# Performance work log

Hardware: AMD Instinct MI355X
Metric: run time of the kernel (lower is better)

The kernel has to match this reference:

```python
import jax, jax.numpy as jnp
import numpy as np

B, N, S, NS = 16, 4096, 512, 32
RADIUS = 0.4
EPS = 1e-5
CHANS = [6, 64, 64, 128]


def setup_inputs() -> dict:
    key = jax.random.key(0)
    ks = jax.random.split(key, 8)
    inp = {
        "xyz": jax.random.normal(ks[0], (B, 3, N), jnp.float32),
        "points": jax.random.normal(ks[1], (B, 3, N), jnp.float32),
    }
    for i in range(3):
        cin, cout = CHANS[i], CHANS[i + 1]
        inp[f"w{i}"] = jax.random.normal(ks[2 + i], (cout, cin), jnp.float32) * (1.0 / np.sqrt(cin))
        inp[f"b{i}"] = jnp.zeros((cout,), jnp.float32)
        inp[f"g{i}"] = jnp.ones((cout,), jnp.float32)
        inp[f"beta{i}"] = jnp.zeros((cout,), jnp.float32)
    return inp


def _fps(xyz):
    # xyz: [B, N, 3] -> indices [B, S] (deterministic start at index 0)
    n = xyz.shape[1]

    def step(carry, _):
        dist, far = carry
        centroid = jnp.take_along_axis(xyz, far[:, None, None], axis=1)  # [B,1,3]
        d = jnp.sum((xyz - centroid) ** 2, -1)                           # [B,N]
        dist = jnp.minimum(dist, d)
        nxt = jnp.argmax(dist, axis=-1).astype(jnp.int32)
        return (dist, nxt), far

    init = (jnp.full((xyz.shape[0], n), 1e10, xyz.dtype), jnp.zeros((xyz.shape[0],), jnp.int32))
    _, idx = jax.lax.scan(step, init, None, length=S)
    return idx.T  # [B, S]


def _query_ball(xyz, new_xyz):
    # xyz: [B,N,3], new_xyz: [B,S,3] -> group indices [B,S,NS]
    n = xyz.shape[1]
    sqr = (jnp.sum(new_xyz ** 2, -1)[:, :, None]
           + jnp.sum(xyz ** 2, -1)[:, None, :]
           - 2.0 * jnp.einsum('bsc,bnc->bsn', new_xyz, xyz))  # [B,S,N]
    grp = jnp.where(sqr <= RADIUS ** 2, jnp.arange(n, dtype=jnp.int32)[None, None, :], n)
    grp = jnp.sort(grp, axis=-1)[:, :, :NS]
    first = grp[:, :, :1]
    return jnp.where(grp == n, first, grp)


_gather = jax.vmap(lambda p, i: p[i])  # p:[N,C], i:[S,NS] -> [S,NS,C]


def _forward(xyz, points, params):
    xyz_t = jnp.transpose(xyz, (0, 2, 1))      # [B,N,3]
    pts_t = jnp.transpose(points, (0, 2, 1))   # [B,N,D]
    fps_idx = _fps(xyz_t)                      # [B,S]
    new_xyz = jnp.take_along_axis(xyz_t, fps_idx[:, :, None], axis=1)  # [B,S,3]
    grp = _query_ball(xyz_t, new_xyz)          # [B,S,NS]
    grouped_xyz = _gather(xyz_t, grp) - new_xyz[:, :, None, :]         # [B,S,NS,3]
    grouped_pts = _gather(pts_t, grp)          # [B,S,NS,D]
    feat = jnp.concatenate([grouped_xyz, grouped_pts], axis=-1)        # [B,S,NS,3+D]
    x = jnp.transpose(feat, (0, 3, 2, 1))      # [B,C,NS,S]
    for (w, b, g, beta) in params:
        x = jnp.einsum('oc,bcns->bons', w, x) + b[None, :, None, None]
        mean = jnp.mean(x, axis=(0, 2, 3), keepdims=True)
        var = jnp.mean((x - mean) ** 2, axis=(0, 2, 3), keepdims=True)
        x = (x - mean) * jax.lax.rsqrt(var + EPS)
        x = jax.nn.relu(x * g[None, :, None, None] + beta[None, :, None, None])
    new_points = jnp.max(x, axis=2)            # [B, C_out, S]
    return jnp.transpose(new_xyz, (0, 2, 1)), new_points


def reference(xyz, points, w0, b0, g0, beta0, w1, b1, g1, beta1, w2, b2, g2, beta2):
    params = [(w0, b0, g0, beta0), (w1, b1, g1, beta1), (w2, b2, g2, beta2)]
    return _forward(xyz, points, params)
```

## Files before the change

kernel.cpp:

```cpp
#include <hip/hip_runtime.h>
#include <math.h>

#define BB 16
#define NN 4096
#define SS 512
#define KK 32
#define NPIX (BB*SS*KK)
#define NGRP (BB*SS)

static constexpr float R2F  = (float)0.16000000000000003;
static constexpr float EPSF = 1e-5f;

constexpr size_t OFF_NXYZ = 0;
constexpr size_t OFF_GRP  = 98304;
constexpr size_t OFF_P1   = 98304 + 1048576;
constexpr size_t OFF_P2   = OFF_P1 + 32768;
constexpr size_t OFF_P3   = OFF_P2 + 32768;
constexpr size_t OFF_MR1  = OFF_P3 + 65536;
constexpr size_t OFF_MR2  = OFF_MR1 + 512;
constexpr size_t OFF_MR3  = OFF_MR2 + 512;
constexpr size_t OFF_Z3   = 2*1024*1024;
constexpr size_t Z3SZ     = (size_t)NPIX*128*4;

#define DPP_FMAX(v, ctrl) { int _t = __builtin_amdgcn_update_dpp(              \
      __float_as_int(v), __float_as_int(v), ctrl, 0xf, 0xf, false);            \
      v = fmaxf(v, __int_as_float(_t)); }
#define DPP_UMIN(v, ctrl) { unsigned _t = (unsigned)__builtin_amdgcn_update_dpp( \
      (int)(v), (int)(v), ctrl, 0xf, 0xf, false);                              \
      v = (v < _t ? v : _t); }

__global__ __launch_bounds__(256) void fps_kernel(const float* __restrict__ xyz,
        float* __restrict__ out0, float* __restrict__ nxyz){
  const int b = blockIdx.x;
  const float* xb = xyz + (size_t)b*3*NN;
  __shared__ float4 pt4[NN];
  __shared__ __align__(16) unsigned long long skey[2][4];
  __shared__ int hist[SS];
  const int t = threadIdx.x;
  const int lane = t & 63, wv = t >> 6;
  float rx[16], ry[16], rz[16], rd[16];
#pragma unroll
  for (int j=0;j<16;j++){
    int i = t + 256*j;
    float x = xb[i], y = xb[NN+i], z = xb[2*NN+i];
    rx[j]=x; ry[j]=y; rz[j]=z;
    pt4[i] = make_float4(x,y,z,0.0f);
    rd[j]=1e10f;
  }
  __syncthreads();
  int far = 0;
  for (int s=0;s<SS;s++){
    const int buf = s & 1;
    float4 c = pt4[far];
    if (t==0) hist[s] = far;
    float bv = -1.0f;
#pragma unroll
    for (int j=0;j<16;j++){
      float dx=__fsub_rn(rx[j],c.x), dy=__fsub_rn(ry[j],c.y), dz=__fsub_rn(rz[j],c.z);
      float d2=__fadd_rn(__fadd_rn(__fmul_rn(dx,dx),__fmul_rn(dy,dy)),__fmul_rn(dz,dz));
      float nd=fminf(rd[j],d2);
      rd[j]=nd;
      bv = fmaxf(bv, nd);
    }
    DPP_FMAX(bv,0x111); DPP_FMAX(bv,0x112); DPP_FMAX(bv,0x114);
    DPP_FMAX(bv,0x118); DPP_FMAX(bv,0x142); DPP_FMAX(bv,0x143);
    const float vmax = __int_as_float(__builtin_amdgcn_readlane(__float_as_int(bv), 63));
    unsigned cand = 0xFFFFFFFFu;
#pragma unroll
    for (int j=15;j>=0;j--) if (rd[j]==vmax) cand = (unsigned)(t+256*j);
    DPP_UMIN(cand,0x111); DPP_UMIN(cand,0x112); DPP_UMIN(cand,0x114);
    DPP_UMIN(cand,0x118); DPP_UMIN(cand,0x142); DPP_UMIN(cand,0x143);
    if (lane==63){
      skey[buf][wv] = ((unsigned long long)(unsigned)__float_as_int(vmax) << 32)
                    | (unsigned)(~cand);
    }
    __syncthreads();
    unsigned long long k0=skey[buf][0], k1=skey[buf][1], k2=skey[buf][2], k3=skey[buf][3];
    unsigned long long m01 = (k0>k1)?k0:k1, m23 = (k2>k3)?k2:k3;
    unsigned long long m   = (m01>m23)?m01:m23;
    far = (int)(~(unsigned)(m & 0xFFFFFFFFull));
  }
  __syncthreads();
  for (int s=t;s<SS;s+=256){
    int idx = hist[s];
    float4 c = pt4[idx];
    int gid = b*SS + s;
    nxyz[gid*3+0]=c.x; nxyz[gid*3+1]=c.y; nxyz[gid*3+2]=c.z;
    out0[(b*3+0)*SS+s]=c.x; out0[(b*3+1)*SS+s]=c.y; out0[(b*3+2)*SS+s]=c.z;
  }
}

__global__ __launch_bounds__(256) void ball_kernel(const float* __restrict__ xyz,
        const float* __restrict__ nxyz, int* __restrict__ grp){
  const int gw   = (blockIdx.x*256 + threadIdx.x) >> 6;
  const int lane = threadIdx.x & 63;
  if (gw >= NGRP) return;
  const int b = gw / SS;
  const float* xb = xyz + (size_t)b*3*NN;
  const float nx=nxyz[gw*3+0], ny=nxyz[gw*3+1], nz=nxyz[gw*3+2];
  const float sn = __fadd_rn(__fadd_rn(__fmul_rn(nx,nx),__fmul_rn(ny,ny)),__fmul_rn(nz,nz));
  int cnt=0, first=-1;
  int* g = grp + (size_t)gw*KK;
  for (int c=0;c<NN/64 && cnt<KK;c++){
    int i=c*64+lane;
    float x=xb[i], y=xb[NN+i], z=xb[2*NN+i];
    float sxx=__fadd_rn(__fadd_rn(__fmul_rn(x,x),__fmul_rn(y,y)),__fmul_rn(z,z));
    float dot=__fadd_rn(__fadd_rn(__fmul_rn(nx,x),__fmul_rn(ny,y)),__fmul_rn(nz,z));
    float sqr=__fsub_rn(__fadd_rn(sn,sxx),__fmul_rn(2.0f,dot));
    bool m = (sqr <= R2F);
    unsigned long long mask = __ballot(m);
    if (m){
      int pos = cnt + __popcll(mask & ((1ull<<lane)-1ull));
      if (pos < KK) g[pos] = i;
    }
    if (first<0 && mask) first = c*64 + (__ffsll((long long)mask) - 1);
    cnt += __popcll(mask);
  }
  if (cnt < KK && lane >= cnt && lane < KK) g[lane] = first;
}

__global__ void finalize_kernel(const double* __restrict__ part, float* __restrict__ mr, int C){
  int o = threadIdx.x;
  if (o < C){
    double s1=0.0, s2=0.0;
    for (int k=0;k<32;k++){ s1 += part[o*32+k]; s2 += part[(C+o)*32+k]; }
    const double n = (double)NPIX;
    double mean = s1/n;
    double var  = s2/n - mean*mean;
    mr[2*o]   = (float)mean;
    mr[2*o+1] = (float)(1.0/sqrt(var + (double)EPSF));
  }
}

constexpr int XIN = 0;
constexpr int W0F = 408;
constexpr int B0F = 792;
constexpr int W1F = 856;
constexpr int B1F = 4952;
constexpr int XBF = 5016;
constexpr int SRF = 9368;
constexpr int W2F = 9624;
constexpr int B2F = 17816;
constexpr int SM_SMALL = 9624;
constexpr int SM_BIG   = 17944;

template<int STAGE, bool STZ3>
__global__ __launch_bounds__(256,2) void mlp_kernel(
    const float* __restrict__ xyz, const float* __restrict__ pts,
    const float* __restrict__ nxyz, const int* __restrict__ grp,
    const float* __restrict__ w0, const float* __restrict__ b0,
    const float* __restrict__ mr1, const float* __restrict__ g0, const float* __restrict__ be0,
    const float* __restrict__ w1, const float* __restrict__ b1,
    const float* __restrict__ mr2, const float* __restrict__ g1, const float* __restrict__ be1,
    const float* __restrict__ w2, const float* __restrict__ b2,
    const float* __restrict__ mr3, const float* __restrict__ g2, const float* __restrict__ be2,
    double* __restrict__ part, float* __restrict__ out1, float* __restrict__ z3w)
{
  __shared__ float sm[(STAGE>=3)? SM_BIG : SM_SMALL];
  const int t   = threadIdx.x;
  const int blk = blockIdx.x;
  const int tx  = t & 15, ty = t >> 4;
  const int p0  = blk*64;
  const int slot = blk & 31;

  sm[SRF + t] = 0.0f;

  for (int i=t;i<384;i+=256){ int o=i/6, c=i-o*6; sm[W0F + c*64 + o] = w0[i]; }
  if (t<64) sm[B0F+t] = b0[t];
  if constexpr (STAGE>=2){
    for (int i=t;i<4096;i+=256){ int o=i&63, c=i>>6; sm[W1F + c*64 + o] = w1[o*64+c]; }
    if (t<64) sm[B1F+t] = b1[t];
  }
  if constexpr (STAGE>=3){
    for (int i=t;i<8192;i+=256){ int o=i&127, c=i>>7; sm[W2F + c*128 + o] = w2[o*64+c]; }
    if (t<128) sm[B2F+t] = b2[t];
  }
  for (int i=t;i<384;i+=256){
    int c=i>>6, px=i&63, p=p0+px, gid=p>>5, bb=p>>14;
    int idx = grp[p];
    float v;
    if (c<3) v = __fsub_rn(xyz[(size_t)bb*3*NN + c*NN + idx], nxyz[gid*3+c]);
    else     v = pts[(size_t)bb*3*NN + (c-3)*NN + idx];
    sm[XIN + c*68 + px] = v;
  }
  __syncthreads();

  float z[4][4];
#pragma unroll
  for (int i=0;i<4;i++)
#pragma unroll
    for (int j=0;j<4;j++) z[i][j]=0.0f;
#pragma unroll
  for (int k=0;k<6;k++){
    float4 xv = *(const float4*)&sm[XIN + k*68 + ty*4];
    float4 wv = *(const float4*)&sm[W0F + k*64 + tx*4];
    const float xs[4]={xv.x,xv.y,xv.z,xv.w};
    const float wsv[4]={wv.x,wv.y,wv.z,wv.w};
#pragma unroll
    for (int i=0;i<4;i++)
#pragma unroll
      for (int j=0;j<4;j++) z[i][j] = fmaf(xs[i], wsv[j], z[i][j]);
  }
#pragma unroll
  for (int i=0;i<4;i++)
#pragma unroll
    for (int j=0;j<4;j++) z[i][j] = __fadd_rn(z[i][j], sm[B0F + tx*4 + j]);

  if constexpr (STAGE==1){
#pragma unroll
    for (int j=0;j<4;j++){
      float s1=0.0f, s2=0.0f;
#pragma unroll
      for (int i=0;i<4;i++){ s1 = __fadd_rn(s1, z[i][j]); s2 = fmaf(z[i][j], z[i][j], s2); }
      atomicAdd(&sm[SRF + (tx*4+j)*2    ], s1);
      atomicAdd(&sm[SRF + (tx*4+j)*2 + 1], s2);
    }
    __syncthreads();
    if (t<128){ int ch=t>>1, m=t&1;
      atomicAdd(part + (size_t)((m? 64+ch : ch)*32 + slot), (double)sm[SRF+t]);
    }
    return;
  }

  if constexpr (STAGE>=2){
#pragma unroll
    for (int j=0;j<4;j++){
      int ch = tx*4+j;
      float m=mr1[2*ch], r=mr1[2*ch+1], gg=g0[ch], bt=be0[ch];
      float4 o;
      o.x = fmaxf(fmaf(__fmul_rn(__fsub_rn(z[0][j],m),r), gg, bt), 0.0f);
      o.y = fmaxf(fmaf(__fmul_rn(__fsub_rn(z[1][j],m),r), gg, bt), 0.0f);
      o.z = fmaxf(fmaf(__fmul_rn(__fsub_rn(z[2][j],m),r), gg, bt), 0.0f);
      o.w = fmaxf(fmaf(__fmul_rn(__fsub_rn(z[3][j],m),r), gg, bt), 0.0f);
      *(float4*)&sm[XBF + ch*68 + ty*4] = o;
    }
    __syncthreads();

#pragma unroll
    for (int i=0;i<4;i++)
#pragma unroll
      for (int j=0;j<4;j++) z[i][j]=0.0f;
#pragma unroll 8
    for (int k=0;k<64;k++){
      float4 xv = *(const float4*)&sm[XBF + k*68 + ty*4];
      float4 wv = *(const float4*)&sm[W1F + k*64 + tx*4];
      const float xs[4]={xv.x,xv.y,xv.z,xv.w};
      const float wsv[4]={wv.x,wv.y,wv.z,wv.w};
#pragma unroll
      for (int i=0;i<4;i++)
#pragma unroll
        for (int j=0;j<4;j++) z[i][j] = fmaf(xs[i], wsv[j], z[i][j]);
    }
#pragma unroll
    for (int i=0;i<4;i++)
#pragma unroll
      for (int j=0;j<4;j++) z[i][j] = __fadd_rn(z[i][j], sm[B1F + tx*4 + j]);

    if constexpr (STAGE==2){
#pragma unroll
      for (int j=0;j<4;j++){
        float s1=0.0f, s2=0.0f;
#pragma unroll
        for (int i=0;i<4;i++){ s1 = __fadd_rn(s1, z[i][j]); s2 = fmaf(z[i][j], z[i][j], s2); }
        atomicAdd(&sm[SRF + (tx*4+j)*2    ], s1);
        atomicAdd(&sm[SRF + (tx*4+j)*2 + 1], s2);
      }
      __syncthreads();
      if (t<128){ int ch=t>>1, m=t&1;
        atomicAdd(part + (size_t)((m? 64+ch : ch)*32 + slot), (double)sm[SRF+t]);
      }
      return;
    }
  }

  if constexpr (STAGE>=3){
    __syncthreads();
#pragma unroll
    for (int j=0;j<4;j++){
      int ch = tx*4+j;
      float m=mr2[2*ch], r=mr2[2*ch+1], gg=g1[ch], bt=be1[ch];
      float4 o;
      o.x = fmaxf(fmaf(__fmul_rn(__fsub_rn(z[0][j],m),r), gg, bt), 0.0f);
      o.y = fmaxf(fmaf(__fmul_rn(__fsub_rn(z[1][j],m),r), gg, bt), 0.0f);
      o.z = fmaxf(fmaf(__fmul_rn(__fsub_rn(z[2][j],m),r), gg, bt), 0.0f);
      o.w = fmaxf(fmaf(__fmul_rn(__fsub_rn(z[3][j],m),r), gg, bt), 0.0f);
      *(float4*)&sm[XBF + ch*68 + ty*4] = o;
    }
    __syncthreads();

    float a3[4][8];
#pragma unroll
    for (int i=0;i<4;i++)
#pragma unroll
      for (int j=0;j<8;j++) a3[i][j]=0.0f;
#pragma unroll 4
    for (int k=0;k<64;k++){
      float4 xv  = *(const float4*)&sm[XBF + k*68  + ty*4];
      float4 wv0 = *(const float4*)&sm[W2F + k*128 + tx*4];
      float4 wv1 = *(const float4*)&sm[W2F + k*128 + 64 + tx*4];
      const float xs[4]={xv.x,xv.y,xv.z,xv.w};
      const float wsv[8]={wv0.x,wv0.y,wv0.z,wv0.w, wv1.x,wv1.y,wv1.z,wv1.w};
#pragma unroll
      for (int i=0;i<4;i++)
#pragma unroll
        for (int j=0;j<8;j++) a3[i][j] = fmaf(xs[i], wsv[j], a3[i][j]);
    }
#pragma unroll
    for (int i=0;i<4;i++)
#pragma unroll
      for (int j=0;j<8;j++){
        int ch = (j<4)? (tx*4+j) : (64+tx*4+(j-4));
        a3[i][j] = __fadd_rn(a3[i][j], sm[B2F + ch]);
      }

    if constexpr (STAGE==3){
      if constexpr (STZ3){
#pragma unroll
        for (int i=0;i<4;i++){
          size_t p = (size_t)(p0 + ty*4 + i)*128;
          *(float4*)&z3w[p + tx*4]      = make_float4(a3[i][0],a3[i][1],a3[i][2],a3[i][3]);
          *(float4*)&z3w[p + 64 + tx*4] = make_float4(a3[i][4],a3[i][5],a3[i][6],a3[i][7]);
        }
      }
#pragma unroll
      for (int j=0;j<8;j++){
        int ch = (j<4)? (tx*4+j) : (64+tx*4+(j-4));
        float s1=0.0f, s2=0.0f;
#pragma unroll
        for (int i=0;i<4;i++){ s1 = __fadd_rn(s1, a3[i][j]); s2 = fmaf(a3[i][j], a3[i][j], s2); }
        atomicAdd(&sm[SRF + ch*2    ], s1);
        atomicAdd(&sm[SRF + ch*2 + 1], s2);
      }
      __syncthreads();
      { int ch=t>>1, m=t&1;
        atomicAdd(part + (size_t)((m? 128+ch : ch)*32 + slot), (double)sm[SRF+t]);
      }
      return;
    }

    if constexpr (STAGE==4){
      const int grp_l = ty>>3;
      unsigned* omax = (unsigned*)sm;
#pragma unroll
      for (int j=0;j<8;j++){
        int ch = (j<4)? (tx*4+j) : (64+tx*4+(j-4));
        float m=mr3[2*ch], r=mr3[2*ch+1], gg=g2[ch], bt=be2[ch];
        float vmax=0.0f;
#pragma unroll
        for (int i=0;i<4;i++){
          float v = fmaxf(fmaf(__fmul_rn(__fsub_rn(a3[i][j],m),r), gg, bt), 0.0f);
          vmax = fmaxf(vmax, v);
        }
        atomicMax(&omax[SRF + grp_l*128 + ch], __float_as_uint(vmax));
      }
      __syncthreads();
      { int g = t>>7, o = t&127;
        int gid = blk*2 + g, bb = gid>>9, s = gid&511;
        out1[((size_t)(bb*128+o))*512 + s] = __uint_as_float(omax[SRF + t]);
      }
    }
  }
}

__global__ __launch_bounds__(256) void maxpool_kernel(const float* __restrict__ z3,
        const float* __restrict__ mr3, const float* __restrict__ g2,
        const float* __restrict__ be2, float* __restrict__ out1){
  const int t = threadIdx.x;
  const int g = blockIdx.x*2 + (t>>7);
  const int o = t & 127;
  const int bb = g >> 9, s = g & 511;
  const float* zp = z3 + (size_t)g*KK*128 + o;
  float m=mr3[2*o], r=mr3[2*o+1], gg=g2[o], bt=be2[o];
  float mx = 0.0f;
#pragma unroll 8
  for (int k=0;k<KK;k++){
    float v = fmaxf(fmaf(__fmul_rn(__fsub_rn(zp[(size_t)k*128],m),r), gg, bt), 0.0f);
    mx = fmaxf(mx, v);
  }
  out1[((size_t)(bb*128+o))*SS + s] = mx;
}

extern "C" void kernel_launch(void* const* d_in, const int* in_sizes, int n_in,
                              void* d_out, int out_size, void* d_ws, size_t ws_size,
                              hipStream_t stream){
  const float* xyz = (const float*)d_in[0];
  const float* pts = (const float*)d_in[1];
  const float* w0  = (const float*)d_in[2];  const float* b0  = (const float*)d_in[3];
  const float* g0  = (const float*)d_in[4];  const float* be0 = (const float*)d_in[5];
  const float* w1  = (const float*)d_in[6];  const float* b1  = (const float*)d_in[7];
  const float* g1  = (const float*)d_in[8];  const float* be1 = (const float*)d_in[9];
  const float* w2  = (const float*)d_in[10]; const float* b2  = (const float*)d_in[11];
  const float* g2  = (const float*)d_in[12]; const float* be2 = (const float*)d_in[13];

  float* out  = (float*)d_out;
  float* out1 = out + BB*3*SS;
  char*  ws   = (char*)d_ws;

  float*  nxyz = (float*)(ws + OFF_NXYZ);
  int*    grp  = (int*)  (ws + OFF_GRP);
  double* p1   = (double*)(ws + OFF_P1);
  double* p2   = (double*)(ws + OFF_P2);
  double* p3   = (double*)(ws + OFF_P3);
  float*  mr1  = (float*)(ws + OFF_MR1);
  float*  mr2  = (float*)(ws + OFF_MR2);
  float*  mr3  = (float*)(ws + OFF_MR3);
  float*  z3w  = (float*)(ws + OFF_Z3);

  const bool stz3 = (ws_size >= OFF_Z3 + Z3SZ);

  hipMemsetAsync(ws + OFF_P1, 0, 32768+32768+65536, stream);

  fps_kernel <<<BB, 256, 0, stream>>>(xyz, out, nxyz);
  ball_kernel<<<NGRP*64/256, 256, 0, stream>>>(xyz, nxyz, grp);

#define MLP_ARGS xyz, pts, nxyz, grp, w0, b0, mr1, g0, be0, w1, b1, mr2, g1, be1, w2, b2, mr3, g2, be2
  mlp_kernel<1,false><<<NPIX/64, 256, 0, stream>>>(MLP_ARGS, p1, out1, z3w);
  finalize_kernel<<<1,128,0,stream>>>(p1, mr1, 64);
  mlp_kernel<2,false><<<NPIX/64, 256, 0, stream>>>(MLP_ARGS, p2, out1, z3w);
  finalize_kernel<<<1,128,0,stream>>>(p2, mr2, 64);
  if (stz3){
    mlp_kernel<3,true><<<NPIX/64, 256, 0, stream>>>(MLP_ARGS, p3, out1, z3w);
    finalize_kernel<<<1,128,0,stream>>>(p3, mr3, 128);
    maxpool_kernel<<<NGRP/2, 256, 0, stream>>>(z3w, mr3, g2, be2, out1);
  } else {
    mlp_kernel<3,false><<<NPIX/64, 256, 0, stream>>>(MLP_ARGS, p3, out1, z3w);
    finalize_kernel<<<1,128,0,stream>>>(p3, mr3, 128);
    mlp_kernel<4,false><<<NPIX/64, 256, 0, stream>>>(MLP_ARGS, p3, out1, z3w);
  }
#undef MLP_ARGS
}
```

Before: 854.5 us.

## Cache layer-2 activations for stage 3 and pack two FPS batches per block

Stage 2 of the MLP now writes its pre-BN layer-2 outputs to a workspace buffer, and stage 3 reads them back instead of regathering inputs and recomputing layers 1 and 2. Separately, the FPS kernel runs two batches per 512-thread block, halving the block count. The stage-3 change swaps redundant compute and weight loads for about 64 MB of extra global writes and reads. It only activates when the workspace is large enough. The FPS change shares barriers across both batches, and the 128 KB of float4 shared memory per block may limit scheduling.

New measurement: 913.9 us. 6.9% more time.

```diff
diff --git a/kernel.cpp b/kernel.cpp
--- a/kernel.cpp
+++ b/kernel.cpp
@@ -21,6 +21,10 @@
 constexpr size_t OFF_MR3  = OFF_MR2 + 512;
 constexpr size_t OFF_Z3   = 2*1024*1024;
 constexpr size_t Z3SZ     = (size_t)NPIX*128*4;
+constexpr size_t OFF_Z2   = OFF_Z3 + Z3SZ;
+constexpr size_t Z2SZ     = (size_t)NPIX*64*4;
+constexpr size_t NEED_Z3  = OFF_Z3 + Z3SZ;
+constexpr size_t NEED_Z2  = OFF_Z2 + Z2SZ;
 
 #define DPP_FMAX(v, ctrl) { int _t = __builtin_amdgcn_update_dpp(              \
       __float_as_int(v), __float_as_int(v), ctrl, 0xf, 0xf, false);            \
@@ -29,30 +33,33 @@
       (int)(v), (int)(v), ctrl, 0xf, 0xf, false);                              \
       v = (v < _t ? v : _t); }
 
-__global__ __launch_bounds__(256) void fps_kernel(const float* __restrict__ xyz,
+__global__ __launch_bounds__(512) void fps_kernel(const float* __restrict__ xyz,
         float* __restrict__ out0, float* __restrict__ nxyz){
-  const int b = blockIdx.x;
+  const int t    = threadIdx.x;
+  const int half = t >> 8;
+  const int tt   = t & 255;
+  const int b    = blockIdx.x*2 + half;
   const float* xb = xyz + (size_t)b*3*NN;
-  __shared__ float4 pt4[NN];
-  __shared__ __align__(16) unsigned long long skey[2][4];
-  __shared__ int hist[SS];
-  const int t = threadIdx.x;
-  const int lane = t & 63, wv = t >> 6;
+  __shared__ float4 pt4[2][NN];
+  __shared__ __align__(16) unsigned long long skey[2][2][4];
+  __shared__ int hist[2][SS];
+  const int lane = t & 63;
+  const int wv   = (t >> 6) & 3;
   float rx[16], ry[16], rz[16], rd[16];
 #pragma unroll
   for (int j=0;j<16;j++){
-    int i = t + 256*j;
+    int i = tt + 256*j;
     float x = xb[i], y = xb[NN+i], z = xb[2*NN+i];
     rx[j]=x; ry[j]=y; rz[j]=z;
-    pt4[i] = make_float4(x,y,z,0.0f);
+    pt4[half][i] = make_float4(x,y,z,0.0f);
     rd[j]=1e10f;
   }
   __syncthreads();
   int far = 0;
   for (int s=0;s<SS;s++){
     const int buf = s & 1;
-    float4 c = pt4[far];
-    if (t==0) hist[s] = far;
+    float4 c = pt4[half][far];
+    if (tt==0) hist[half][s] = far;
     float bv = -1.0f;
 #pragma unroll
     for (int j=0;j<16;j++){
@@ -67,23 +74,24 @@
     const float vmax = __int_as_float(__builtin_amdgcn_readlane(__float_as_int(bv), 63));
     unsigned cand = 0xFFFFFFFFu;
 #pragma unroll
-    for (int j=15;j>=0;j--) if (rd[j]==vmax) cand = (unsigned)(t+256*j);
+    for (int j=15;j>=0;j--) if (rd[j]==vmax) cand = (unsigned)(tt+256*j);
     DPP_UMIN(cand,0x111); DPP_UMIN(cand,0x112); DPP_UMIN(cand,0x114);
     DPP_UMIN(cand,0x118); DPP_UMIN(cand,0x142); DPP_UMIN(cand,0x143);
     if (lane==63){
-      skey[buf][wv] = ((unsigned long long)(unsigned)__float_as_int(vmax) << 32)
-                    | (unsigned)(~cand);
+      skey[half][buf][wv] = ((unsigned long long)(unsigned)__float_as_int(vmax) << 32)
+                          | (unsigned)(~cand);
     }
     __syncthreads();
-    unsigned long long k0=skey[buf][0], k1=skey[buf][1], k2=skey[buf][2], k3=skey[buf][3];
+    unsigned long long k0=skey[half][buf][0], k1=skey[half][buf][1],
+                       k2=skey[half][buf][2], k3=skey[half][buf][3];
     unsigned long long m01 = (k0>k1)?k0:k1, m23 = (k2>k3)?k2:k3;
     unsigned long long m   = (m01>m23)?m01:m23;
     far = (int)(~(unsigned)(m & 0xFFFFFFFFull));
   }
   __syncthreads();
-  for (int s=t;s<SS;s+=256){
-    int idx = hist[s];
-    float4 c = pt4[idx];
+  for (int s=tt;s<SS;s+=256){
+    int idx = hist[half][s];
+    float4 c = pt4[half][idx];
     int gid = b*SS + s;
     nxyz[gid*3+0]=c.x; nxyz[gid*3+1]=c.y; nxyz[gid*3+2]=c.z;
     out0[(b*3+0)*SS+s]=c.x; out0[(b*3+1)*SS+s]=c.y; out0[(b*3+2)*SS+s]=c.z;
@@ -144,7 +152,7 @@
 constexpr int SM_SMALL = 9624;
 constexpr int SM_BIG   = 17944;
 
-template<int STAGE, bool STZ3>
+template<int STAGE, bool STZ3, bool Z2IO>
 __global__ __launch_bounds__(256,2) void mlp_kernel(
     const float* __restrict__ xyz, const float* __restrict__ pts,
     const float* __restrict__ nxyz, const int* __restrict__ grp,
@@ -154,7 +162,8 @@
     const float* __restrict__ mr2, const float* __restrict__ g1, const float* __restrict__ be1,
     const float* __restrict__ w2, const float* __restrict__ b2,
     const float* __restrict__ mr3, const float* __restrict__ g2, const float* __restrict__ be2,
-    double* __restrict__ part, float* __restrict__ out1, float* __restrict__ z3w)
+    double* __restrict__ part, float* __restrict__ out1,
+    float* __restrict__ z2w, float* __restrict__ z3w)
 {
   __shared__ float sm[(STAGE>=3)? SM_BIG : SM_SMALL];
   const int t   = threadIdx.x;
@@ -162,67 +171,76 @@
   const int tx  = t & 15, ty = t >> 4;
   const int p0  = blk*64;
   const int slot = blk & 31;
+  constexpr bool SKIP12 = (STAGE==3 && Z2IO);
 
   sm[SRF + t] = 0.0f;
 
-  for (int i=t;i<384;i+=256){ int o=i/6, c=i-o*6; sm[W0F + c*64 + o] = w0[i]; }
-  if (t<64) sm[B0F+t] = b0[t];
-  if constexpr (STAGE>=2){
-    for (int i=t;i<4096;i+=256){ int o=i&63, c=i>>6; sm[W1F + c*64 + o] = w1[o*64+c]; }
-    if (t<64) sm[B1F+t] = b1[t];
+  if constexpr (!SKIP12){
+    for (int i=t;i<384;i+=256){ int o=i/6, c=i-o*6; sm[W0F + c*64 + o] = w0[i]; }
+    if (t<64) sm[B0F+t] = b0[t];
+    if constexpr (STAGE>=2){
+      for (int i=t;i<4096;i+=256){ int o=i&63, c=i>>6; sm[W1F + c*64 + o] = w1[o*64+c]; }
+      if (t<64) sm[B1F+t] = b1[t];
+    }
+    for (int i=t;i<384;i+=256){
+      int c=i>>6, px=i&63, p=p0+px, gid=p>>5, bb=p>>14;
+      int idx = grp[p];
+      float v;
+      if (c<3) v = __fsub_rn(xyz[(size_t)bb*3*NN + c*NN + idx], nxyz[gid*3+c]);
+      else     v = pts[(size_t)bb*3*NN + (c-3)*NN + idx];
+      sm[XIN + c*68 + px] = v;
+    }
   }
   if constexpr (STAGE>=3){
     for (int i=t;i<8192;i+=256){ int o=i&127, c=i>>7; sm[W2F + c*128 + o] = w2[o*64+c]; }
     if (t<128) sm[B2F+t] = b2[t];
   }
-  for (int i=t;i<384;i+=256){
-    int c=i>>6, px=i&63, p=p0+px, gid=p>>5, bb=p>>14;
-    int idx = grp[p];
-    float v;
-    if (c<3) v = __fsub_rn(xyz[(size_t)bb*3*NN + c*NN + idx], nxyz[gid*3+c]);
-    else     v = pts[(size_t)bb*3*NN + (c-3)*NN + idx];
-    sm[XIN + c*68 + px] = v;
-  }
   __syncthreads();
 
   float z[4][4];
-#pragma unroll
-  for (int i=0;i<4;i++)
-#pragma unroll
-    for (int j=0;j<4;j++) z[i][j]=0.0f;
-#pragma unroll
-  for (int k=0;k<6;k++){
-    float4 xv = *(const float4*)&sm[XIN + k*68 + ty*4];
-    float4 wv = *(const float4*)&sm[W0F + k*64 + tx*4];
-    const float xs[4]={xv.x,xv.y,xv.z,xv.w};
-    const float wsv[4]={wv.x,wv.y,wv.z,wv.w};
-#pragma unroll
-    for (int i=0;i<4;i++)
-#pragma unroll
-      for (int j=0;j<4;j++) z[i][j] = fmaf(xs[i], wsv[j], z[i][j]);
-  }
-#pragma unroll
-  for (int i=0;i<4;i++)
-#pragma unroll
-    for (int j=0;j<4;j++) z[i][j] = __fadd_rn(z[i][j], sm[B0F + tx*4 + j]);
-
-  if constexpr (STAGE==1){
-#pragma unroll
-    for (int j=0;j<4;j++){
-      float s1=0.0f, s2=0.0f;
-#pragma unroll
-      for (int i=0;i<4;i++){ s1 = __fadd_rn(s1, z[i][j]); s2 = fmaf(z[i][j], z[i][j], s2); }
-      atomicAdd(&sm[SRF + (tx*4+j)*2    ], s1);
-      atomicAdd(&sm[SRF + (tx*4+j)*2 + 1], s2);
-    }
-    __syncthreads();
-    if (t<128){ int ch=t>>1, m=t&1;
-      atomicAdd(part + (size_t)((m? 64+ch : ch)*32 + slot), (double)sm[SRF+t]);
-    }
-    return;
-  }
-
-  if constexpr (STAGE>=2){
+  if constexpr (SKIP12){
+#pragma unroll
+    for (int i=0;i<4;i++){
+      float4 v = *(const float4*)&z2w[(size_t)(p0 + ty*4 + i)*64 + tx*4];
+      z[i][0]=v.x; z[i][1]=v.y; z[i][2]=v.z; z[i][3]=v.w;
+    }
+  } else {
+#pragma unroll
+    for (int i=0;i<4;i++)
+#pragma unroll
+      for (int j=0;j<4;j++) z[i][j]=0.0f;
+#pragma unroll
+    for (int k=0;k<6;k++){
+      float4 xv = *(const float4*)&sm[XIN + k*68 + ty*4];
+      float4 wv = *(const float4*)&sm[W0F + k*64 + tx*4];
+      const float xs[4]={xv.x,xv.y,xv.z,xv.w};
+      const float wsv[4]={wv.x,wv.y,wv.z,wv.w};
+#pragma unroll
+      for (int i=0;i<4;i++)
+#pragma unroll
+        for (int j=0;j<4;j++) z[i][j] = fmaf(xs[i], wsv[j], z[i][j]);
+    }
+#pragma unroll
+    for (int i=0;i<4;i++)
+#pragma unroll
+      for (int j=0;j<4;j++) z[i][j] = __fadd_rn(z[i][j], sm[B0F + tx*4 + j]);
+
+    if constexpr (STAGE==1){
+#pragma unroll
+      for (int j=0;j<4;j++){
+        float s1=0.0f, s2=0.0f;
+#pragma unroll
+        for (int i=0;i<4;i++){ s1 = __fadd_rn(s1, z[i][j]); s2 = fmaf(z[i][j], z[i][j], s2); }
+        atomicAdd(&sm[SRF + (tx*4+j)*2    ], s1);
+        atomicAdd(&sm[SRF + (tx*4+j)*2 + 1], s2);
+      }
+      __syncthreads();
+      if (t<128){ int ch=t>>1, m=t&1;
+        atomicAdd(part + (size_t)((m? 64+ch : ch)*32 + slot), (double)sm[SRF+t]);
+      }
+      return;
+    }
+
 #pragma unroll
     for (int j=0;j<4;j++){
       int ch = tx*4+j;
@@ -257,6 +275,12 @@
       for (int j=0;j<4;j++) z[i][j] = __fadd_rn(z[i][j], sm[B1F + tx*4 + j]);
 
     if constexpr (STAGE==2){
+      if constexpr (Z2IO){
+#pragma unroll
+        for (int i=0;i<4;i++)
+          *(float4*)&z2w[(size_t)(p0 + ty*4 + i)*64 + tx*4]
+              = make_float4(z[i][0], z[i][1], z[i][2], z[i][3]);
+      }
 #pragma unroll
       for (int j=0;j<4;j++){
         float s1=0.0f, s2=0.0f;
@@ -405,27 +429,27 @@
   float*  mr2  = (float*)(ws + OFF_MR2);
   float*  mr3  = (float*)(ws + OFF_MR3);
   float*  z3w  = (float*)(ws + OFF_Z3);
-
-  const bool stz3 = (ws_size >= OFF_Z3 + Z3SZ);
+  float*  z2w  = (float*)(ws + OFF_Z2);
+
+  const bool stz3 = (ws_size >= NEED_Z3);
+  const bool stz2 = (ws_size >= NEED_Z2);
 
   hipMemsetAsync(ws + OFF_P1, 0, 32768+32768+65536, stream);
 
-  fps_kernel <<<BB, 256, 0, stream>>>(xyz, out, nxyz);
+  fps_kernel <<<BB/2, 512, 0, stream>>>(xyz, out, nxyz);
   ball_kernel<<<NGRP*64/256, 256, 0, stream>>>(xyz, nxyz, grp);
 
 #define MLP_ARGS xyz, pts, nxyz, grp, w0, b0, mr1, g0, be0, w1, b1, mr2, g1, be1, w2, b2, mr3, g2, be2
-  mlp_kernel<1,false><<<NPIX/64, 256, 0, stream>>>(MLP_ARGS, p1, out1, z3w);
+  mlp_kernel<1,false,false><<<NPIX/64, 256, 0, stream>>>(MLP_ARGS, p1, out1, z2w, z3w);
   finalize_kernel<<<1,128,0,stream>>>(p1, mr1, 64);
-  mlp_kernel<2,false><<<NPIX/64, 256, 0, stream>>>(MLP_ARGS, p2, out1, z3w);
+  if (stz2) mlp_kernel<2,false,true ><<<NPIX/64, 256, 0, stream>>>(MLP_ARGS, p2, out1, z2w, z3w);
+  else      mlp_kernel<2,false,false><<<NPIX/64, 256, 0, stream>>>(MLP_ARGS, p2, out1, z2w, z3w);
   finalize_kernel<<<1,128,0,stream>>>(p2, mr2, 64);
-  if (stz3){
-    mlp_kernel<3,true><<<NPIX/64, 256, 0, stream>>>(MLP_ARGS, p3, out1, z3w);
-    finalize_kernel<<<1,128,0,stream>>>(p3, mr3, 128);
-    maxpool_kernel<<<NGRP/2, 256, 0, stream>>>(z3w, mr3, g2, be2, out1);
-  } else {
-    mlp_kernel<3,false><<<NPIX/64, 256, 0, stream>>>(MLP_ARGS, p3, out1, z3w);
-    finalize_kernel<<<1,128,0,stream>>>(p3, mr3, 128);
-    mlp_kernel<4,false><<<NPIX/64, 256, 0, stream>>>(MLP_ARGS, p3, out1, z3w);
-  }
+  if (stz2)      mlp_kernel<3,true ,true ><<<NPIX/64, 256, 0, stream>>>(MLP_ARGS, p3, out1, z2w, z3w);
+  else if (stz3) mlp_kernel<3,true ,false><<<NPIX/64, 256, 0, stream>>>(MLP_ARGS, p3, out1, z2w, z3w);
+  else           mlp_kernel<3,false,false><<<NPIX/64, 256, 0, stream>>>(MLP_ARGS, p3, out1, z2w, z3w);
+  finalize_kernel<<<1,128,0,stream>>>(p3, mr3, 128);
+  if (stz3) maxpool_kernel<<<NGRP/2, 256, 0, stream>>>(z3w, mr3, g2, be2, out1);
+  else      mlp_kernel<4,false,false><<<NPIX/64, 256, 0, stream>>>(MLP_ARGS, p3, out1, z2w, z3w);
 #undef MLP_ARGS
 }
```
